# Optimization experiments

Measured on AMD Instinct MI355X. Metric: run time of the kernel, lower is better.

The kernel has to match this reference:

```python
import jax, jax.numpy as jnp
import numpy as np
from jax import lax

N_ITER = 5   # self.n from __init__
K = 2.0      # self.k from __init__

def _avg_pool2(x):
    B, C, H, W = x.shape
    return x.reshape(B, C, H // 2, 2, W // 2, 2).mean(axis=(3, 5))

def _max_pool2(x):
    B, C, H, W = x.shape
    return x.reshape(B, C, H // 2, 2, W // 2, 2).max(axis=(3, 5))

def _box_dilate(x):
    # 3x3 all-ones conv, stride 1, padding 1, single channel
    k = jnp.ones((1, 1, 3, 3), x.dtype)
    return lax.conv_general_dilated(x, k, (1, 1), ((1, 1), (1, 1)),
                                    dimension_numbers=('NCHW', 'OIHW', 'NCHW'))

def setup_inputs() -> dict:
    key = jax.random.key(0)
    k1, k2, k3, k4, k5, k6, k7 = jax.random.split(key, 7)
    B, Cf, Hf, Wf = 8, 256, 128, 128
    H, W = 512, 512
    F_in = jax.random.normal(k1, (B, Cf, Hf, Wf), jnp.float32)
    img_p = jax.random.uniform(k2, (B, 3, H, W), jnp.float32)
    m = jax.random.randint(k3, (B, 1, H, W), 0, 2).astype(jnp.float32)
    mask = jnp.tile(m, (1, 3, 1, 1))
    gamma_w = jax.random.normal(k4, (Cf, 3), jnp.float32) * 0.1
    gamma_b = jax.random.normal(k5, (Cf,), jnp.float32) * 0.1
    beta_w = jax.random.normal(k6, (Cf, 3), jnp.float32) * 0.1
    beta_b = jax.random.normal(k7, (Cf,), jnp.float32) * 0.1
    return {"F_in": F_in, "img_p": img_p, "mask": mask,
            "gamma_w": gamma_w, "gamma_b": gamma_b,
            "beta_w": beta_w, "beta_b": beta_b,
            "n_ds": 2, "n": 2}

def reference(F_in, img_p, mask, gamma_w, gamma_b, beta_w, beta_b, n_ds, n):
    for _ in range(n_ds):
        img_p = _avg_pool2(img_p)
        mask = _max_pool2(mask)
    mask = mask[:, :1]                         # torch.chunk(..., 3)[0]
    D_h = mask
    msk = (mask == 1.0)
    for i in range(1, N_ITER + 1):
        D_h = _box_dilate(D_h)
        tmp = (D_h > 0) & (~msk)               # newly reached pixels
        msk = msk | tmp
        mask = jnp.where(tmp, 1.0 / K ** i, mask)
        D_h = mask
    gamma_hp = jnp.einsum('bchw,oc->bohw', img_p, gamma_w) + gamma_b[None, :, None, None]
    beta_hp = jnp.einsum('bchw,oc->bohw', img_p, beta_w) + beta_b[None, :, None, None]
    if n == 1:
        gamma_hd = lax.stop_gradient(gamma_hp) * D_h
        beta_hd = lax.stop_gradient(beta_hp) * D_h
    else:
        gamma_hd = gamma_hp * D_h
        beta_hd = beta_hp * D_h
    mean = jnp.mean(F_in)
    var = jnp.var(F_in, ddof=1)                # torch.var default unbiased
    F_norm = (F_in - mean) / jnp.sqrt(var ** 2 + 1e-5)  # var**2 as in source
    return F_norm * gamma_hd + beta_hd
```

## Files before the change

### kernel.cpp

```cpp
#include <hip/hip_runtime.h>
#include <math.h>

constexpr int B  = 8;
constexpr int CF = 256;
constexpr int HF = 128;
constexpr int WF = 128;
constexpr int HP = 512;
constexpr int WP = 512;
constexpr long long NTOT = (long long)B * CF * HF * WF;

typedef float f4 __attribute__((ext_vector_type(4)));

constexpr size_t STATS_OFF = 0;
constexpr size_t DH_OFF    = 256;
constexpr size_t IMG_OFF   = DH_OFF + (size_t)B * HF * WF * sizeof(float);
constexpr size_t PART_OFF  = IMG_OFF + (size_t)B * 3 * HF * WF * sizeof(float);

constexpr int RBLOCKS  = 2048;
constexpr int RTHREADS = 256;
constexpr int PBLOCKS  = 512;
constexpr long long CH_S = (long long)RBLOCKS * RTHREADS * 4;

__global__ void __launch_bounds__(RTHREADS) k_reduce_pool(
        const float* __restrict__ F,
        const float* __restrict__ img, const float* __restrict__ mask,
        float* __restrict__ img_ds, float* __restrict__ mds,
        double2* __restrict__ part) {
    __shared__ double ls[4], lq[4];
    const int bid = blockIdx.x;
    if (bid < PBLOCKS) {
        int t = bid * RTHREADS + threadIdx.x;
        int w = t & (WF - 1);
        int h = (t >> 7) & (HF - 1);
        int b = t >> 14;
        for (int c = 0; c < 3; ++c) {
            const float* p = img + (((b * 3 + c) * HP + h * 4) * WP + w * 4);
            float s = 0.0f;
            for (int r = 0; r < 4; ++r) {
                f4 v = *(const f4*)(p + r * WP);
                s += v.x + v.y + v.z + v.w;
            }
            img_ds[((b * 3 + c) << 14) | (h << 7) | w] = s * 0.0625f;
        }
        const float* pm = mask + (((b * 3) * HP + h * 4) * WP + w * 4);
        float m = 0.0f;
        for (int r = 0; r < 4; ++r) {
            f4 v = *(const f4*)(pm + r * WP);
            m = fmaxf(m, fmaxf(fmaxf(v.x, v.y), fmaxf(v.z, v.w)));
        }
        mds[t] = m;
        return;
    }
    const int rb = bid - PBLOCKS;
    const long long tid = (long long)rb * RTHREADS + threadIdx.x;
    const float* p = F + tid * 4;
    f4 v[16];
#pragma unroll
    for (int k = 0; k < 16; ++k)
        v[k] = *(const f4*)(p + k * CH_S);
    double s0 = 0, s1 = 0, s2 = 0, s3 = 0;
    double q0 = 0, q1 = 0, q2 = 0, q3 = 0;
#pragma unroll
    for (int k = 0; k < 16; k += 4) {
        {
            f4 w = v[k + 0];
            s0 += (double)((w.x + w.y) + (w.z + w.w));
            q0 += (double)((w.x * w.x + w.y * w.y) + (w.z * w.z + w.w * w.w));
        }
        {
            f4 w = v[k + 1];
            s1 += (double)((w.x + w.y) + (w.z + w.w));
            q1 += (double)((w.x * w.x + w.y * w.y) + (w.z * w.z + w.w * w.w));
        }
        {
            f4 w = v[k + 2];
            s2 += (double)((w.x + w.y) + (w.z + w.w));
            q2 += (double)((w.x * w.x + w.y * w.y) + (w.z * w.z + w.w * w.w));
        }
        {
            f4 w = v[k + 3];
            s3 += (double)((w.x + w.y) + (w.z + w.w));
            q3 += (double)((w.x * w.x + w.y * w.y) + (w.z * w.z + w.w * w.w));
        }
    }
    double s = (s0 + s1) + (s2 + s3);
    double q = (q0 + q1) + (q2 + q3);
    for (int off = 32; off > 0; off >>= 1) {
        s += __shfl_down(s, off);
        q += __shfl_down(q, off);
    }
    int lane = threadIdx.x & 63, wv = threadIdx.x >> 6;
    if (lane == 0) { ls[wv] = s; lq[wv] = q; }
    __syncthreads();
    if (threadIdx.x == 0) {
        double S_ = 0.0, Q_ = 0.0;
        for (int w = 0; w < 4; ++w) { S_ += ls[w]; Q_ += lq[w]; }
        part[rb] = make_double2(S_, Q_);
    }
}

__global__ void __launch_bounds__(1024) k_dilate_stats(float* __restrict__ Dh,
                                                       const double2* __restrict__ part,
                                                       float* __restrict__ stats) {
    if (blockIdx.x == 8) {
        double s = 0.0, q = 0.0;
        for (int i = threadIdx.x; i < RBLOCKS; i += 1024) {
            double2 p = part[i];
            s += p.x; q += p.y;
        }
        for (int off = 32; off > 0; off >>= 1) {
            s += __shfl_down(s, off);
            q += __shfl_down(q, off);
        }
        __shared__ double ls[16], lq[16];
        int lane = threadIdx.x & 63, wv = threadIdx.x >> 6;
        if (lane == 0) { ls[wv] = s; lq[wv] = q; }
        __syncthreads();
        if (threadIdx.x == 0) {
            double S_ = 0.0, Q_ = 0.0;
            for (int w = 0; w < 16; ++w) { S_ += ls[w]; Q_ += lq[w]; }
            double mean = S_ / (double)NTOT;
            double var  = (Q_ - (double)NTOT * mean * mean) / (double)(NTOT - 1);
            stats[0] = (float)mean;
            stats[1] = (float)(1.0 / sqrt(var * var + 1e-5));
        }
        return;
    }
    __shared__ float M[HF * WF];
    const int b = blockIdx.x;
    float* img = Dh + b * HF * WF;
    for (int i = threadIdx.x; i < HF * WF; i += 1024) M[i] = img[i];
    __syncthreads();
    float invk = 1.0f;
    for (int it = 1; it <= 5; ++it) {
        invk *= 0.5f;
        unsigned nf = 0;
        for (int j = 0; j < 16; ++j) {
            int p = threadIdx.x + j * 1024;
            if (M[p] != 0.0f) continue;
            int h = p >> 7, w = p & 127;
            bool any = false;
            for (int dh = -1; dh <= 1; ++dh) {
                int hh = h + dh;
                if (hh < 0 || hh >= HF) continue;
                for (int dw = -1; dw <= 1; ++dw) {
                    int ww = w + dw;
                    if (ww < 0 || ww >= WF) continue;
                    any = any || (M[(hh << 7) | ww] > 0.0f);
                }
            }
            if (any) nf |= (1u << j);
        }
        __syncthreads();
        for (int j = 0; j < 16; ++j)
            if (nf & (1u << j)) M[threadIdx.x + j * 1024] = invk;
        __syncthreads();
    }
    for (int i = threadIdx.x; i < HF * WF; i += 1024) img[i] = M[i];
}

constexpr int CGRP = 8;
__global__ void __launch_bounds__(256) k_final(const float* __restrict__ F,
                        const float* __restrict__ img_ds,
                        const float* __restrict__ Dh,
                        const float* __restrict__ gw, const float* __restrict__ gb,
                        const float* __restrict__ bw, const float* __restrict__ bb,
                        const float* __restrict__ stats,
                        float* __restrict__ out) {
    const int ihh = blockIdx.x & 15;
    const int icg = (blockIdx.x >> 4) & 31;
    const int ib  = blockIdx.x >> 9;
    const int iw  = threadIdx.x & 31;
    const int ih  = (ihh << 3) | (threadIdx.x >> 5);
    const int w   = iw * 4;
    const int c0  = icg * CGRP;

    const float meanf = stats[0];
    const float rstd  = stats[1];

    const int pixoff = (ih << 7) | w;
    const int pix = (ib << 14) | pixoff;
    f4 D = *(const f4*)(Dh + pix);
    const float* ip = img_ds + ((size_t)ib * 3 << 14);
    f4 R  = *(const f4*)(ip + ((0 << 14) | pixoff));
    f4 G  = *(const f4*)(ip + ((1 << 14) | pixoff));
    f4 Bl = *(const f4*)(ip + ((2 << 14) | pixoff));

    const size_t fbase = (((size_t)(ib * CF + c0)) << 14) + pixoff;

    f4 Fv[CGRP];
#pragma unroll
    for (int j = 0; j < CGRP; ++j)
        Fv[j] = *(const f4*)(F + fbase + ((size_t)j << 14));

#pragma unroll
    for (int j = 0; j < CGRP; ++j) {
        const int c = c0 + j;
        float g0 = gw[c * 3], g1 = gw[c * 3 + 1], g2 = gw[c * 3 + 2], gbi = gb[c];
        float b0 = bw[c * 3], b1 = bw[c * 3 + 1], b2 = bw[c * 3 + 2], bbi = bb[c];
        f4 o;
        {
            float gam = (R.x * g0 + G.x * g1 + Bl.x * g2 + gbi) * D.x;
            float bet = (R.x * b0 + G.x * b1 + Bl.x * b2 + bbi) * D.x;
            o.x = (Fv[j].x - meanf) * rstd * gam + bet;
        }
        {
            float gam = (R.y * g0 + G.y * g1 + Bl.y * g2 + gbi) * D.y;
            float bet = (R.y * b0 + G.y * b1 + Bl.y * b2 + bbi) * D.y;
            o.y = (Fv[j].y - meanf) * rstd * gam + bet;
        }
        {
            float gam = (R.z * g0 + G.z * g1 + Bl.z * g2 + gbi) * D.z;
            float bet = (R.z * b0 + G.z * b1 + Bl.z * b2 + bbi) * D.z;
            o.z = (Fv[j].z - meanf) * rstd * gam + bet;
        }
        {
            float gam = (R.w * g0 + G.w * g1 + Bl.w * g2 + gbi) * D.w;
            float bet = (R.w * b0 + G.w * b1 + Bl.w * b2 + bbi) * D.w;
            o.w = (Fv[j].w - meanf) * rstd * gam + bet;
        }
        __builtin_nontemporal_store(o, (f4*)(out + fbase + ((size_t)j << 14)));
    }
}

extern "C" void kernel_launch(void* const* d_in, const int* in_sizes, int n_in,
                              void* d_out, int out_size, void* d_ws, size_t ws_size,
                              hipStream_t stream) {
    const float* F_in  = (const float*)d_in[0];
    const float* img_p = (const float*)d_in[1];
    const float* mask  = (const float*)d_in[2];
    const float* gw    = (const float*)d_in[3];
    const float* gb    = (const float*)d_in[4];
    const float* bw    = (const float*)d_in[5];
    const float* bb    = (const float*)d_in[6];
    float* out = (float*)d_out;

    float*   stats  = (float*)((char*)d_ws + STATS_OFF);
    float*   Dh     = (float*)((char*)d_ws + DH_OFF);
    float*   img_ds = (float*)((char*)d_ws + IMG_OFF);
    double2* part   = (double2*)((char*)d_ws + PART_OFF);

    k_reduce_pool<<<PBLOCKS + RBLOCKS, RTHREADS, 0, stream>>>(
        F_in, img_p, mask, img_ds, Dh, part);
    k_dilate_stats<<<B + 1, 1024, 0, stream>>>(Dh, part, stats);
    k_final<<<(int)(NTOT / (4 * CGRP) / 256), 256, 0, stream>>>(
        F_in, img_ds, Dh, gw, gb, bw, bb, stats, out);
}
```

Before: 304.0 us.

## Replace iterative dilation kernel with closed-form Chebyshev distance fused into final kernel

Drops the separate dilation/stats kernel. Each zero mask pixel's weight is now computed directly in the final kernel from the Chebyshev distance to the nearest nonzero pixel within radius 5, mapped to 2^-d. The final stats reduction is folded into every final block, and the final grid shrinks so each block handles four row groups. The F reduction changes from strided to contiguous chunks, and output stores become regular instead of nontemporal. This removes a serial single-block-per-batch kernel and a launch, but adds redundant 11x11 neighbourhood scans per zero pixel, repeated per channel-group block, plus a redundant partial-sum reduction in every block.

```diff
diff --git a/kernel.cpp b/kernel.cpp
--- a/kernel.cpp
+++ b/kernel.cpp
@@ -11,7 +11,6 @@
 
 typedef float f4 __attribute__((ext_vector_type(4)));
 
-constexpr size_t STATS_OFF = 0;
 constexpr size_t DH_OFF    = 256;
 constexpr size_t IMG_OFF   = DH_OFF + (size_t)B * HF * WF * sizeof(float);
 constexpr size_t PART_OFF  = IMG_OFF + (size_t)B * 3 * HF * WF * sizeof(float);
@@ -19,7 +18,7 @@
 constexpr int RBLOCKS  = 2048;
 constexpr int RTHREADS = 256;
 constexpr int PBLOCKS  = 512;
-constexpr long long CH_S = (long long)RBLOCKS * RTHREADS * 4;
+constexpr int RCHUNK   = 16384;
 
 __global__ void __launch_bounds__(RTHREADS) k_reduce_pool(
         const float* __restrict__ F,
@@ -52,12 +51,11 @@
         return;
     }
     const int rb = bid - PBLOCKS;
-    const long long tid = (long long)rb * RTHREADS + threadIdx.x;
-    const float* p = F + tid * 4;
+    const float* p = F + (size_t)rb * RCHUNK + threadIdx.x * 4;
     f4 v[16];
 #pragma unroll
     for (int k = 0; k < 16; ++k)
-        v[k] = *(const f4*)(p + k * CH_S);
+        v[k] = *(const f4*)(p + k * (RTHREADS * 4));
     double s0 = 0, s1 = 0, s2 = 0, s3 = 0;
     double q0 = 0, q1 = 0, q2 = 0, q3 = 0;
 #pragma unroll
@@ -99,127 +97,121 @@
     }
 }
 
-__global__ void __launch_bounds__(1024) k_dilate_stats(float* __restrict__ Dh,
-                                                       const double2* __restrict__ part,
-                                                       float* __restrict__ stats) {
-    if (blockIdx.x == 8) {
+__device__ __forceinline__ float dt_val(const float* __restrict__ mds,
+                                        int ib, int h, int w) {
+    int best = 6;
+    for (int dh = -5; dh <= 5; ++dh) {
+        int hh = h + dh;
+        if ((unsigned)hh >= (unsigned)HF) continue;
+        for (int dw = -5; dw <= 5; ++dw) {
+            int ww = w + dw;
+            if ((unsigned)ww >= (unsigned)WF) continue;
+            if (mds[(ib << 14) | (hh << 7) | ww] != 0.0f) {
+                int ad = abs(dh) > abs(dw) ? abs(dh) : abs(dw);
+                best = best < ad ? best : ad;
+            }
+        }
+    }
+    const float tbl[7] = {1.0f, 0.5f, 0.25f, 0.125f, 0.0625f, 0.03125f, 0.0f};
+    return tbl[best];
+}
+
+constexpr int CGRP = 8;
+__global__ void __launch_bounds__(256) k_final(const float* __restrict__ F,
+                        const float* __restrict__ img_ds,
+                        const float* __restrict__ mds,
+                        const float* __restrict__ gw, const float* __restrict__ gb,
+                        const float* __restrict__ bw, const float* __restrict__ bb,
+                        const double2* __restrict__ part,
+                        float* __restrict__ out) {
+    __shared__ double ls[4], lq[4];
+    __shared__ float s_stats[2];
+    {
         double s = 0.0, q = 0.0;
-        for (int i = threadIdx.x; i < RBLOCKS; i += 1024) {
-            double2 p = part[i];
+        for (int k = 0; k < 8; ++k) {
+            double2 p = part[k * 256 + threadIdx.x];
             s += p.x; q += p.y;
         }
         for (int off = 32; off > 0; off >>= 1) {
             s += __shfl_down(s, off);
             q += __shfl_down(q, off);
         }
-        __shared__ double ls[16], lq[16];
         int lane = threadIdx.x & 63, wv = threadIdx.x >> 6;
         if (lane == 0) { ls[wv] = s; lq[wv] = q; }
         __syncthreads();
         if (threadIdx.x == 0) {
-            double S_ = 0.0, Q_ = 0.0;
-            for (int w = 0; w < 16; ++w) { S_ += ls[w]; Q_ += lq[w]; }
+            double S_ = (ls[0] + ls[1]) + (ls[2] + ls[3]);
+            double Q_ = (lq[0] + lq[1]) + (lq[2] + lq[3]);
             double mean = S_ / (double)NTOT;
             double var  = (Q_ - (double)NTOT * mean * mean) / (double)(NTOT - 1);
-            stats[0] = (float)mean;
-            stats[1] = (float)(1.0 / sqrt(var * var + 1e-5));
-        }
-        return;
-    }
-    __shared__ float M[HF * WF];
-    const int b = blockIdx.x;
-    float* img = Dh + b * HF * WF;
-    for (int i = threadIdx.x; i < HF * WF; i += 1024) M[i] = img[i];
-    __syncthreads();
-    float invk = 1.0f;
-    for (int it = 1; it <= 5; ++it) {
-        invk *= 0.5f;
-        unsigned nf = 0;
-        for (int j = 0; j < 16; ++j) {
-            int p = threadIdx.x + j * 1024;
-            if (M[p] != 0.0f) continue;
-            int h = p >> 7, w = p & 127;
-            bool any = false;
-            for (int dh = -1; dh <= 1; ++dh) {
-                int hh = h + dh;
-                if (hh < 0 || hh >= HF) continue;
-                for (int dw = -1; dw <= 1; ++dw) {
-                    int ww = w + dw;
-                    if (ww < 0 || ww >= WF) continue;
-                    any = any || (M[(hh << 7) | ww] > 0.0f);
-                }
-            }
-            if (any) nf |= (1u << j);
+            s_stats[0] = (float)mean;
+            s_stats[1] = (float)(1.0 / sqrt(var * var + 1e-5));
         }
         __syncthreads();
-        for (int j = 0; j < 16; ++j)
-            if (nf & (1u << j)) M[threadIdx.x + j * 1024] = invk;
-        __syncthreads();
-    }
-    for (int i = threadIdx.x; i < HF * WF; i += 1024) img[i] = M[i];
-}
-
-constexpr int CGRP = 8;
-__global__ void __launch_bounds__(256) k_final(const float* __restrict__ F,
-                        const float* __restrict__ img_ds,
-                        const float* __restrict__ Dh,
-                        const float* __restrict__ gw, const float* __restrict__ gb,
-                        const float* __restrict__ bw, const float* __restrict__ bb,
-                        const float* __restrict__ stats,
-                        float* __restrict__ out) {
-    const int ihh = blockIdx.x & 15;
-    const int icg = (blockIdx.x >> 4) & 31;
-    const int ib  = blockIdx.x >> 9;
-    const int iw  = threadIdx.x & 31;
-    const int ih  = (ihh << 3) | (threadIdx.x >> 5);
-    const int w   = iw * 4;
-    const int c0  = icg * CGRP;
-
-    const float meanf = stats[0];
-    const float rstd  = stats[1];
-
-    const int pixoff = (ih << 7) | w;
-    const int pix = (ib << 14) | pixoff;
-    f4 D = *(const f4*)(Dh + pix);
+    }
+    const float meanf = s_stats[0];
+    const float rstd  = s_stats[1];
+
+    const int ihh4 = blockIdx.x & 3;
+    const int icg  = (blockIdx.x >> 2) & 31;
+    const int ib   = blockIdx.x >> 7;
+    const int iw   = threadIdx.x & 31;
+    const int w4   = iw * 4;
+    const int c0   = icg * CGRP;
+
     const float* ip = img_ds + ((size_t)ib * 3 << 14);
-    f4 R  = *(const f4*)(ip + ((0 << 14) | pixoff));
-    f4 G  = *(const f4*)(ip + ((1 << 14) | pixoff));
-    f4 Bl = *(const f4*)(ip + ((2 << 14) | pixoff));
-
-    const size_t fbase = (((size_t)(ib * CF + c0)) << 14) + pixoff;
-
-    f4 Fv[CGRP];
-#pragma unroll
-    for (int j = 0; j < CGRP; ++j)
-        Fv[j] = *(const f4*)(F + fbase + ((size_t)j << 14));
-
-#pragma unroll
-    for (int j = 0; j < CGRP; ++j) {
-        const int c = c0 + j;
-        float g0 = gw[c * 3], g1 = gw[c * 3 + 1], g2 = gw[c * 3 + 2], gbi = gb[c];
-        float b0 = bw[c * 3], b1 = bw[c * 3 + 1], b2 = bw[c * 3 + 2], bbi = bb[c];
-        f4 o;
-        {
-            float gam = (R.x * g0 + G.x * g1 + Bl.x * g2 + gbi) * D.x;
-            float bet = (R.x * b0 + G.x * b1 + Bl.x * b2 + bbi) * D.x;
-            o.x = (Fv[j].x - meanf) * rstd * gam + bet;
-        }
-        {
-            float gam = (R.y * g0 + G.y * g1 + Bl.y * g2 + gbi) * D.y;
-            float bet = (R.y * b0 + G.y * b1 + Bl.y * b2 + bbi) * D.y;
-            o.y = (Fv[j].y - meanf) * rstd * gam + bet;
-        }
-        {
-            float gam = (R.z * g0 + G.z * g1 + Bl.z * g2 + gbi) * D.z;
-            float bet = (R.z * b0 + G.z * b1 + Bl.z * b2 + bbi) * D.z;
-            o.z = (Fv[j].z - meanf) * rstd * gam + bet;
-        }
-        {
-            float gam = (R.w * g0 + G.w * g1 + Bl.w * g2 + gbi) * D.w;
-            float bet = (R.w * b0 + G.w * b1 + Bl.w * b2 + bbi) * D.w;
-            o.w = (Fv[j].w - meanf) * rstd * gam + bet;
-        }
-        __builtin_nontemporal_store(o, (f4*)(out + fbase + ((size_t)j << 14)));
+
+    for (int sub = 0; sub < 4; ++sub) {
+        const int ih = ihh4 * 32 + sub * 8 + (threadIdx.x >> 5);
+        const int pixoff = (ih << 7) | w4;
+        const int pix = (ib << 14) | pixoff;
+
+        f4 m4 = *(const f4*)(mds + pix);
+        f4 D;
+        D.x = (m4.x != 0.0f) ? m4.x : dt_val(mds, ib, ih, w4 + 0);
+        D.y = (m4.y != 0.0f) ? m4.y : dt_val(mds, ib, ih, w4 + 1);
+        D.z = (m4.z != 0.0f) ? m4.z : dt_val(mds, ib, ih, w4 + 2);
+        D.w = (m4.w != 0.0f) ? m4.w : dt_val(mds, ib, ih, w4 + 3);
+
+        f4 R  = *(const f4*)(ip + ((0 << 14) | pixoff));
+        f4 G  = *(const f4*)(ip + ((1 << 14) | pixoff));
+        f4 Bl = *(const f4*)(ip + ((2 << 14) | pixoff));
+
+        const size_t fbase = (((size_t)(ib * CF + c0)) << 14) + pixoff;
+
+        f4 Fv[CGRP];
+#pragma unroll
+        for (int j = 0; j < CGRP; ++j)
+            Fv[j] = *(const f4*)(F + fbase + ((size_t)j << 14));
+
+#pragma unroll
+        for (int j = 0; j < CGRP; ++j) {
+            const int c = c0 + j;
+            float g0 = gw[c * 3], g1 = gw[c * 3 + 1], g2 = gw[c * 3 + 2], gbi = gb[c];
+            float b0 = bw[c * 3], b1 = bw[c * 3 + 1], b2 = bw[c * 3 + 2], bbi = bb[c];
+            f4 o;
+            {
+                float gam = (R.x * g0 + G.x * g1 + Bl.x * g2 + gbi) * D.x;
+                float bet = (R.x * b0 + G.x * b1 + Bl.x * b2 + bbi) * D.x;
+                o.x = (Fv[j].x - meanf) * rstd * gam + bet;
+            }
+            {
+                float gam = (R.y * g0 + G.y * g1 + Bl.y * g2 + gbi) * D.y;
+                float bet = (R.y * b0 + G.y * b1 + Bl.y * b2 + bbi) * D.y;
+                o.y = (Fv[j].y - meanf) * rstd * gam + bet;
+            }
+            {
+                float gam = (R.z * g0 + G.z * g1 + Bl.z * g2 + gbi) * D.z;
+                float bet = (R.z * b0 + G.z * b1 + Bl.z * b2 + bbi) * D.z;
+                o.z = (Fv[j].z - meanf) * rstd * gam + bet;
+            }
+            {
+                float gam = (R.w * g0 + G.w * g1 + Bl.w * g2 + gbi) * D.w;
+                float bet = (R.w * b0 + G.w * b1 + Bl.w * b2 + bbi) * D.w;
+                o.w = (Fv[j].w - meanf) * rstd * gam + bet;
+            }
+            *(f4*)(out + fbase + ((size_t)j << 14)) = o;
+        }
     }
 }
 
@@ -235,14 +227,12 @@
     const float* bb    = (const float*)d_in[6];
     float* out = (float*)d_out;
 
-    float*   stats  = (float*)((char*)d_ws + STATS_OFF);
-    float*   Dh     = (float*)((char*)d_ws + DH_OFF);
+    float*   mds    = (float*)((char*)d_ws + DH_OFF);
     float*   img_ds = (float*)((char*)d_ws + IMG_OFF);
     double2* part   = (double2*)((char*)d_ws + PART_OFF);
 
     k_reduce_pool<<<PBLOCKS + RBLOCKS, RTHREADS, 0, stream>>>(
-        F_in, img_p, mask, img_ds, Dh, part);
-    k_dilate_stats<<<B + 1, 1024, 0, stream>>>(Dh, part, stats);
-    k_final<<<(int)(NTOT / (4 * CGRP) / 256), 256, 0, stream>>>(
-        F_in, img_ds, Dh, gw, gb, bw, bb, stats, out);
-}
+        F_in, img_p, mask, img_ds, mds, part);
+    k_final<<<8 * 32 * 4, 256, 0, stream>>>(
+        F_in, img_ds, mds, gw, gb, bw, bb, part, out);
+}
```

New measurement: 305.9 us. Within noise of the previous version (+0.6%).
